# Optimization experiments

Hardware: AMD Instinct MI355X
Metric: run time of the kernel (lower is better)

## Reference

```python
import jax, jax.numpy as jnp
import numpy as np

B, S, D, H, FF = 2, 2048, 1024, 16, 4096
HD = D // H          # head dim = 64
ROT = HD // 2        # rotary dim = dim/(num_heads*2) = 32 (partial rotation)
EPS = 1e-5


def setup_inputs() -> dict:
    key = jax.random.key(0)
    ks = jax.random.split(key, 16)
    std = 0.02
    return {
        "x": jax.random.normal(ks[0], (B, S, D), jnp.float32),
        "mask": jnp.ones((B, 1, 1, S), jnp.int32),
        "wq": jax.random.normal(ks[1], (D, D), jnp.float32) * std,
        "bq": jnp.zeros((D,), jnp.float32),
        "wk": jax.random.normal(ks[2], (D, D), jnp.float32) * std,
        "bk": jnp.zeros((D,), jnp.float32),
        "wv": jax.random.normal(ks[3], (D, D), jnp.float32) * std,
        "bv": jnp.zeros((D,), jnp.float32),
        "wo": jax.random.normal(ks[4], (D, D), jnp.float32) * std,
        "bo": jnp.zeros((D,), jnp.float32),
        "ln1_w": jnp.ones((D,), jnp.float32),
        "ln1_b": jnp.zeros((D,), jnp.float32),
        "ln2_w": jnp.ones((D,), jnp.float32),
        "ln2_b": jnp.zeros((D,), jnp.float32),
        "w1": jax.random.normal(ks[5], (D, FF), jnp.float32) * std,
        "b1": jnp.zeros((FF,), jnp.float32),
        "w2": jax.random.normal(ks[6], (FF, D), jnp.float32) * std,
        "b2": jnp.zeros((D,), jnp.float32),
    }


def _layernorm(x, w, b):
    mu = jnp.mean(x, axis=-1, keepdims=True)
    var = jnp.mean(jnp.square(x - mu), axis=-1, keepdims=True)
    return (x - mu) * jax.lax.rsqrt(var + EPS) * w + b


def _rope(t):
    # t: [B, H, S, HD]; rotate first ROT features, interleaved (GPT-J) pairing
    inv_freq = 1.0 / (10000.0 ** (jnp.arange(0, ROT, 2, dtype=jnp.float32) / ROT))
    ang = jnp.arange(S, dtype=jnp.float32)[:, None] * inv_freq      # [S, ROT//2]
    ang = jnp.repeat(ang, 2, axis=-1)                               # [S, ROT]
    cos, sin = jnp.cos(ang), jnp.sin(ang)
    t_rot, t_pass = t[..., :ROT], t[..., ROT:]
    pr = t_rot.reshape(*t_rot.shape[:-1], ROT // 2, 2)
    rot = jnp.stack([-pr[..., 1], pr[..., 0]], axis=-1).reshape(t_rot.shape)
    return jnp.concatenate([t_rot * cos + rot * sin, t_pass], axis=-1)


def reference(x, mask, wq, bq, wk, bk, wv, bv, wo, bo,
              ln1_w, ln1_b, ln2_w, ln2_b, w1, b1, w2, b2):
    res = x
    h = _layernorm(x, ln1_w, ln1_b)
    q = (h @ wq + bq).reshape(B, S, H, HD).transpose(0, 2, 1, 3)
    k = (h @ wk + bk).reshape(B, S, H, HD).transpose(0, 2, 1, 3)
    v = (h @ wv + bv).reshape(B, S, H, HD).transpose(0, 2, 1, 3)
    q, k = _rope(q), _rope(k)
    score = jnp.einsum('bhqd,bhkd->bhqk', q, k) * (1.0 / np.sqrt(HD))
    score = jnp.where(mask == 0, jnp.float32(-1e9), score)
    attn = jax.nn.softmax(score, axis=-1)
    out = jnp.einsum('bhqk,bhkd->bhqd', attn, v)
    out = out.transpose(0, 2, 1, 3).reshape(B, S, D) @ wo + bo
    x = res + out
    res = x
    h = _layernorm(x, ln2_w, ln2_b)
    h = jax.nn.gelu(h @ w1 + b1, approximate=False) @ w2 + b2
    return res + h
```

## Files before the change

### kernel.cpp

```cpp
#include <hip/hip_runtime.h>
#include <cstdint>
#include <cstddef>


typedef __bf16 bf16;
typedef __bf16 bf16x2 __attribute__((ext_vector_type(2)));
typedef __bf16 bf16x4v __attribute__((ext_vector_type(4)));
typedef __bf16 bf16x8 __attribute__((ext_vector_type(8)));
typedef float  f32x4  __attribute__((ext_vector_type(4)));

#define NB 2
#define NS 2048
#define ND 1024
#define NH 16
#define NHD 64
#define NFF 4096
#define NM (NB*NS)
#define QKSCALE 0.18033688011112042f

typedef uint32_t __attribute__((address_space(1))) gu32_t;
typedef uint32_t __attribute__((address_space(3))) lu32_t;
__device__ __forceinline__ void async_copy16(void* lds, const void* g) {
  __builtin_amdgcn_global_load_lds((gu32_t*)g, (lu32_t*)lds, 16, 0, 0);
}

__device__ __forceinline__ float gelu_f(float x) {
  return 0.5f * x * (1.0f + erff(x * 0.70710678118654752f));
}

__global__ __launch_bounds__(256) void prep_kernel(
    const float* __restrict__ wq, const float* __restrict__ wk,
    const float* __restrict__ wv, const float* __restrict__ wo,
    const float* __restrict__ w1, const float* __restrict__ w2,
    bf16* __restrict__ wqt, bf16* __restrict__ wkt, bf16* __restrict__ wvt,
    bf16* __restrict__ wot, bf16* __restrict__ w1t, bf16* __restrict__ w2t,
    const float* __restrict__ bq, const float* __restrict__ bk,
    const float* __restrict__ bv, float* __restrict__ bcat,
    const int* __restrict__ mask, float* __restrict__ m01f,
    bf16* __restrict__ m01b, float2* __restrict__ rtab,
    const float* __restrict__ x, const float* __restrict__ ln1w,
    const float* __restrict__ ln1b, bf16* __restrict__ h1) {
  int flat = blockIdx.x;
  int t = threadIdx.x;
  if (flat < 12288) {
    __shared__ float tile[32][33];
    const float* W; bf16* Wt; long bx, by; int K, N;
    if (flat < 4096) {
      int which = flat >> 10, r = flat & 1023;
      const float* Ws[4] = {wq, wk, wv, wo};
      bf16* Wts[4] = {wqt, wkt, wvt, wot};
      W = Ws[which]; Wt = Wts[which]; bx = r & 31; by = r >> 5; K = ND; N = ND;
    } else if (flat < 8192) {
      int r = flat - 4096;
      W = w1; Wt = w1t; bx = r & 127; by = r >> 7; K = ND; N = NFF;
    } else {
      int r = flat - 8192;
      W = w2; Wt = w2t; bx = r & 31; by = r >> 5; K = NFF; N = ND;
    }
    int tx = t & 31, ty = t >> 5;
#pragma unroll
    for (int r = 0; r < 4; ++r)
      tile[ty + r*8][tx] = W[(by*32 + ty + r*8) * (long)N + bx*32 + tx];
    __syncthreads();
#pragma unroll
    for (int r = 0; r < 4; ++r)
      Wt[(bx*32 + ty + r*8) * (long)K + by*32 + tx] = (bf16)tile[tx][ty + r*8];
  } else if (flat < 12444) {
    int blk = flat - 12288;
    if (blk < 12) {
      int i = blk * 256 + t;
      bcat[i] = (i < ND) ? bq[i] : ((i < 2*ND) ? bk[i - ND] : bv[i - 2*ND]);
    } else if (blk < 28) {
      int i = (blk - 12) * 256 + t;
      float v = mask[i] ? 1.0f : 0.0f;
      m01f[i] = v;
      m01b[i] = (bf16)v;
    } else {
      int idx = (blk - 28) * 256 + t;
      int s = idx >> 4, i = idx & 15;
      float ang = (float)s * exp2f(-(float)i * (13.287712379549449f / 16.0f));
      float sn, cs;
      sincosf(ang, &sn, &cs);
      rtab[idx] = make_float2(cs, sn);
    }
  } else {
    long row = flat - 12444;
    float4 v = ((const float4*)(x + row*ND))[t];
    float s  = v.x + v.y + v.z + v.w;
    float sq = v.x*v.x + v.y*v.y + v.z*v.z + v.w*v.w;
#pragma unroll
    for (int m = 1; m <= 32; m <<= 1) { s += __shfl_xor(s, m); sq += __shfl_xor(sq, m); }
    __shared__ float ss[4], ssq[4];
    if ((t & 63) == 0) { ss[t>>6] = s; ssq[t>>6] = sq; }
    __syncthreads();
    s  = ss[0] + ss[1] + ss[2] + ss[3];
    sq = ssq[0] + ssq[1] + ssq[2] + ssq[3];
    float mu = s * (1.0f/ND);
    float rs = rsqrtf(sq * (1.0f/ND) - mu*mu + 1e-5f);
    float4 wv4 = ((const float4*)ln1w)[t];
    float4 bv4 = ((const float4*)ln1b)[t];
    bf16x4v o;
    o[0] = (bf16)((v.x-mu)*rs*wv4.x + bv4.x);
    o[1] = (bf16)((v.y-mu)*rs*wv4.y + bv4.y);
    o[2] = (bf16)((v.z-mu)*rs*wv4.z + bv4.z);
    o[3] = (bf16)((v.w-mu)*rs*wv4.w + bv4.w);
    *(bf16x4v*)(h1 + row*ND + t*4) = o;
  }
}

__global__ __launch_bounds__(256) void vtrans_kernel(
    const bf16* __restrict__ v, bf16* __restrict__ vt) {
  __shared__ bf16 t[64][66];
  int st = blockIdx.x, bh = blockIdx.y;
  int b = bh >> 4, h = bh & 15;
  int c = threadIdx.x & 63, rg = threadIdx.x >> 6;
  const bf16* src = v + ((long)b*NS + st*64)*ND + h*64;
#pragma unroll
  for (int i = 0; i < 16; ++i) {
    int r = rg*16 + i;
    t[r][c] = src[(long)r*ND + c];
  }
  __syncthreads();
  bf16* dst = vt + (long)bh*64*NS + st*64;
#pragma unroll
  for (int i = 0; i < 16; ++i) {
    int d = rg*16 + i;
    dst[(long)d*NS + c] = t[c][d];
  }
}

__global__ __launch_bounds__(256) void ln_kernel(
    const float* __restrict__ x, const float* __restrict__ w,
    const float* __restrict__ b, bf16* __restrict__ out) {
  long row = blockIdx.x;
  int t = threadIdx.x;
  float4 v = ((const float4*)(x + row*ND))[t];
  float s  = v.x + v.y + v.z + v.w;
  float sq = v.x*v.x + v.y*v.y + v.z*v.z + v.w*v.w;
#pragma unroll
  for (int m = 1; m <= 32; m <<= 1) { s += __shfl_xor(s, m); sq += __shfl_xor(sq, m); }
  __shared__ float ss[4], ssq[4];
  if ((t & 63) == 0) { ss[t>>6] = s; ssq[t>>6] = sq; }
  __syncthreads();
  s  = ss[0] + ss[1] + ss[2] + ss[3];
  sq = ssq[0] + ssq[1] + ssq[2] + ssq[3];
  float mu = s * (1.0f/ND);
  float rs = rsqrtf(sq * (1.0f/ND) - mu*mu + 1e-5f);
  float4 wv = ((const float4*)w)[t];
  float4 bv = ((const float4*)b)[t];
  bf16x4v o;
  o[0] = (bf16)((v.x-mu)*rs*wv.x + bv.x);
  o[1] = (bf16)((v.y-mu)*rs*wv.y + bv.y);
  o[2] = (bf16)((v.z-mu)*rs*wv.z + bv.z);
  o[3] = (bf16)((v.w-mu)*rs*wv.w + bv.w);
  *(bf16x4v*)(out + row*ND + t*4) = o;
}

__global__ __launch_bounds__(256) void ffn2red_kernel(
    const float* __restrict__ P, const float* __restrict__ y1,
    const float* __restrict__ b2, float* __restrict__ out) {
  const long n4 = (long)NM * ND / 4;
  const float4* p = (const float4*)P;
  const float4* y = (const float4*)y1;
  const float4* bb = (const float4*)b2;
  float4* o = (float4*)out;
  for (long i = (long)blockIdx.x*256 + threadIdx.x; i < n4;
       i += (long)gridDim.x*256) {
    float4 a0 = p[i], a1 = p[i + n4], a2 = p[i + 2*n4], a3 = p[i + 3*n4];
    float4 yv = y[i];
    float4 bv = bb[i & 255];
    float4 r;
    r.x = (a0.x + a1.x) + (a2.x + a3.x) + yv.x + bv.x;
    r.y = (a0.y + a1.y) + (a2.y + a3.y) + yv.y + bv.y;
    r.z = (a0.z + a1.z) + (a2.z + a3.z) + yv.z + bv.z;
    r.w = (a0.w + a1.w) + (a2.w + a3.w) + yv.w + bv.w;
    o[i] = r;
  }
}

template<int EPI>
__global__ __launch_bounds__(512, 2) void gemm256_kernel(
    const bf16* __restrict__ A, const bf16* __restrict__ Bt,
    const float* __restrict__ bias, void* __restrict__ Cout,
    const float2* __restrict__ rtab, const float* __restrict__ m01f,
    int M, int N, int K, int lda, int ldbt) {
  __shared__ __align__(16) bf16 Alds[2][256*64];
  __shared__ __align__(16) bf16 Blds[2][256*64];
  const int tid = threadIdx.x, lane = tid & 63, w = tid >> 6;
  const int fr = lane & 15, kg = lane >> 4;
  const int wr = w >> 2, wc = w & 3;
  const int kz = (EPI == 2) ? blockIdx.z : 0;
  const long kofs = (long)kz * K;

  const int gx = gridDim.x;
  int lin = blockIdx.y * gx + blockIdx.x;
  int nwg = gx * gridDim.y;
  int swz = (lin & 7) * (nwg >> 3) + (lin >> 3);
  const long am0 = (long)(swz / gx) * 256;
  const long bn0 = (long)(swz % gx) * 256;

  const f32x4 fzero = {0.f, 0.f, 0.f, 0.f};
  f32x4 acc[8][4];
#pragma unroll
  for (int m = 0; m < 8; ++m)
#pragma unroll
    for (int n = 0; n < 4; ++n) acc[m][n] = fzero;

  auto stage = [&](int kt, int bufi) {
#pragma unroll
    for (int i = 0; i < 4; ++i) {
      int s = i*512 + tid;
      int r = s >> 3, c = (s & 7) ^ (r & 7);
      async_copy16((char*)&Alds[bufi][0] + i*8192 + w*1024,
                   &A[(am0 + r)*(long)lda + kofs + kt + c*8]);
    }
#pragma unroll
    for (int i = 0; i < 4; ++i) {
      int s = i*512 + tid;
      int r = s >> 3, c = (s & 7) ^ (r & 7);
      async_copy16((char*)&Blds[bufi][0] + i*8192 + w*1024,
                   &Bt[(bn0 + r)*(long)ldbt + kofs + kt + c*8]);
    }
  };

  const int nk = K >> 6;
  stage(0, 0);
  stage(64, 1);
  asm volatile("s_waitcnt vmcnt(8)" ::: "memory");
  __builtin_amdgcn_s_barrier();
  __builtin_amdgcn_sched_barrier(0);

  for (int t = 0; t < nk; ++t) {
    const char* Ab = (const char*)&Alds[t & 1][0];
    const char* Bb = (const char*)&Blds[t & 1][0];
    bf16x8 bfv0[4], bfv1[4], af[4];
#pragma unroll
    for (int n = 0; n < 4; ++n) {
      int r = wc*64 + n*16 + fr;
      bfv0[n] = *(const bf16x8*)(Bb + r*128 + ((kg ^ (r & 7)) << 4));
    }
#pragma unroll
    for (int m = 0; m < 4; ++m) {
      int r = wr*128 + m*16 + fr;
      af[m] = *(const bf16x8*)(Ab + r*128 + ((kg ^ (r & 7)) << 4));
    }
    asm volatile("s_waitcnt lgkmcnt(0)" ::: "memory");
    __builtin_amdgcn_sched_barrier(0);
    __builtin_amdgcn_s_setprio(1);
#pragma unroll
    for (int m = 0; m < 4; ++m)
#pragma unroll
      for (int n = 0; n < 4; ++n)
        acc[m][n] = __builtin_amdgcn_mfma_f32_16x16x32_bf16(af[m], bfv0[n], acc[m][n], 0, 0, 0);
    __builtin_amdgcn_s_setprio(0);
#pragma unroll
    for (int n = 0; n < 4; ++n) {
      int r = wc*64 + n*16 + fr;
      bfv1[n] = *(const bf16x8*)(Bb + r*128 + (((4 + kg) ^ (r & 7)) << 4));
    }
#pragma unroll
    for (int m = 0; m < 4; ++m) {
      int r = wr*128 + m*16 + fr;
      af[m] = *(const bf16x8*)(Ab + r*128 + (((4 + kg) ^ (r & 7)) << 4));
    }
    asm volatile("s_waitcnt lgkmcnt(0)" ::: "memory");
    __builtin_amdgcn_sched_barrier(0);
    __builtin_amdgcn_s_setprio(1);
#pragma unroll
    for (int m = 0; m < 4; ++m)
#pragma unroll
      for (int n = 0; n < 4; ++n)
        acc[m][n] = __builtin_amdgcn_mfma_f32_16x16x32_bf16(af[m], bfv1[n], acc[m][n], 0, 0, 0);
    __builtin_amdgcn_s_setprio(0);
#pragma unroll
    for (int m = 0; m < 4; ++m) {
      int r = wr*128 + (m+4)*16 + fr;
      af[m] = *(const bf16x8*)(Ab + r*128 + ((kg ^ (r & 7)) << 4));
    }
    asm volatile("s_waitcnt lgkmcnt(0)" ::: "memory");
    __builtin_amdgcn_sched_barrier(0);
    __builtin_amdgcn_s_setprio(1);
#pragma unroll
    for (int m = 0; m < 4; ++m)
#pragma unroll
      for (int n = 0; n < 4; ++n)
        acc[m+4][n] = __builtin_amdgcn_mfma_f32_16x16x32_bf16(af[m], bfv0[n], acc[m+4][n], 0, 0, 0);
    __builtin_amdgcn_s_setprio(0);
#pragma unroll
    for (int m = 0; m < 4; ++m) {
      int r = wr*128 + (m+4)*16 + fr;
      af[m] = *(const bf16x8*)(Ab + r*128 + (((4 + kg) ^ (r & 7)) << 4));
    }
    asm volatile("s_waitcnt lgkmcnt(0)" ::: "memory");
    __builtin_amdgcn_sched_barrier(0);
    __builtin_amdgcn_s_setprio(1);
#pragma unroll
    for (int m = 0; m < 4; ++m)
#pragma unroll
      for (int n = 0; n < 4; ++n)
        acc[m+4][n] = __builtin_amdgcn_mfma_f32_16x16x32_bf16(af[m], bfv1[n], acc[m+4][n], 0, 0, 0);
    __builtin_amdgcn_s_setprio(0);

    if (t + 1 == nk) break;
    __builtin_amdgcn_s_barrier();
    __builtin_amdgcn_sched_barrier(0);
    if (t + 2 < nk) {
      stage((t + 2) * 64, t & 1);
      asm volatile("s_waitcnt vmcnt(8)" ::: "memory");
    } else {
      asm volatile("s_waitcnt vmcnt(0)" ::: "memory");
    }
    __builtin_amdgcn_s_barrier();
    __builtin_amdgcn_sched_barrier(0);
  }

  const int rbase = kg * 4;
  const int region = (int)(bn0 >> 10);
#pragma unroll
  for (int m = 0; m < 8; ++m) {
#pragma unroll
    for (int n = 0; n < 4; ++n) {
      long col = bn0 + wc*64 + n*16 + fr;
      float bia = (EPI == 2) ? 0.0f : bias[col];
#pragma unroll
      for (int j = 0; j < 4; ++j) {
        long row = am0 + wr*128 + m*16 + rbase + j;
        float val = acc[m][n][j] + bia;
        if (EPI == 1) {
          ((bf16*)Cout)[row * N + col] = (bf16)gelu_f(val);
        } else if (EPI == 2) {
          ((float*)Cout)[((long)kz * NM + row) * N + col] = val;
        } else {
          long cv = col & 1023;
          if (region <= 1) {
            float pval = __shfl_xor(val, 1);
            if (n < 2) {
              float2 cs = rtab[((row & (NS-1)) << 4) | ((n*16 + fr) >> 1)];
              val = (fr & 1) ? val*cs.x + pval*cs.y : val*cs.x - pval*cs.y;
            }
            if (region == 0) val *= QKSCALE;
          } else {
            val *= m01f[row];
          }
          ((bf16*)Cout)[(long)region * (NM*(long)ND) + row * ND + cv] = (bf16)val;
        }
      }
    }
  }
}

__global__ __launch_bounds__(512, 1) void gemm128x8_kernel(
    const bf16* __restrict__ A, const bf16* __restrict__ Bt,
    const float* __restrict__ bias, const float* __restrict__ res,
    float* __restrict__ Cout, int M, int N, int K) {
  __shared__ __align__(16) bf16 Alds[4][128*64];
  __shared__ __align__(16) bf16 Blds[4][128*64];
  const int tid = threadIdx.x, lane = tid & 63, w = tid >> 6;
  const int fr = lane & 15, kg = lane >> 4;
  const int wr = w >> 1, wc = w & 1;

  const int gx = gridDim.x;
  int lin = blockIdx.y * gx + blockIdx.x;
  int nwg = gx * gridDim.y;
  int swz = (lin & 7) * (nwg >> 3) + (lin >> 3);
  const long am0 = (long)(swz / gx) * 128;
  const long bn0 = (long)(swz % gx) * 128;

  const f32x4 fzero = {0.f, 0.f, 0.f, 0.f};
  f32x4 acc[2][4];
#pragma unroll
  for (int m = 0; m < 2; ++m)
#pragma unroll
    for (int n = 0; n < 4; ++n) acc[m][n] = fzero;

  auto stage = [&](int kt, int bufi) {
#pragma unroll
    for (int i = 0; i < 2; ++i) {
      int s = i*512 + tid;
      int r = s >> 3, c = (s & 7) ^ (r & 7);
      async_copy16((char*)&Alds[bufi][0] + i*8192 + w*1024,
                   &A[(am0 + r)*K + kt + c*8]);
      async_copy16((char*)&Blds[bufi][0] + i*8192 + w*1024,
                   &Bt[(bn0 + r)*K + kt + c*8]);
    }
  };

  const int nk = K >> 6;
  stage(0, 0);
  stage(64, 1);
  asm volatile("s_waitcnt vmcnt(4)" ::: "memory");
  __builtin_amdgcn_s_barrier();
  __builtin_amdgcn_sched_barrier(0);

  for (int t = 0; t < nk; ++t) {
    const int cur = t & 3;
    if (t + 2 < nk) stage((t + 2) * 64, (t + 2) & 3);
    const char* Ab = (const char*)&Alds[cur][0];
    const char* Bb = (const char*)&Blds[cur][0];
    bf16x8 af[2][2], bfv[2][4];
#pragma unroll
    for (int kk = 0; kk < 2; ++kk) {
#pragma unroll
      for (int m = 0; m < 2; ++m) {
        int r = wr*32 + m*16 + fr;
        af[kk][m] = *(const bf16x8*)(Ab + r*128 + (((kk*4 + kg) ^ (r & 7)) << 4));
      }
#pragma unroll
      for (int n = 0; n < 4; ++n) {
        int r = wc*64 + n*16 + fr;
        bfv[kk][n] = *(const bf16x8*)(Bb + r*128 + (((kk*4 + kg) ^ (r & 7)) << 4));
      }
    }
    asm volatile("s_waitcnt lgkmcnt(0)" ::: "memory");
    __builtin_amdgcn_sched_barrier(0);
    __builtin_amdgcn_s_setprio(1);
#pragma unroll
    for (int kk = 0; kk < 2; ++kk)
#pragma unroll
      for (int m = 0; m < 2; ++m)
#pragma unroll
        for (int n = 0; n < 4; ++n)
          acc[m][n] = __builtin_amdgcn_mfma_f32_16x16x32_bf16(af[kk][m], bfv[kk][n], acc[m][n], 0, 0, 0);
    __builtin_amdgcn_s_setprio(0);
    if (t + 2 < nk) { asm volatile("s_waitcnt vmcnt(4)" ::: "memory"); }
    else            { asm volatile("s_waitcnt vmcnt(0)" ::: "memory"); }
    __builtin_amdgcn_s_barrier();
    __builtin_amdgcn_sched_barrier(0);
  }

  const int rbase = kg * 4;
#pragma unroll
  for (int m = 0; m < 2; ++m) {
#pragma unroll
    for (int n = 0; n < 4; ++n) {
      long col = bn0 + wc*64 + n*16 + fr;
      float bia = bias[col];
#pragma unroll
      for (int j = 0; j < 4; ++j) {
        long row = am0 + wr*32 + m*16 + rbase + j;
        Cout[row * N + col] = acc[m][n][j] + bia + res[row * N + col];
      }
    }
  }
}

__global__ __launch_bounds__(512) void attn_kernel(
    const bf16* __restrict__ q, const bf16* __restrict__ k,
    const bf16* __restrict__ vt, const bf16* __restrict__ m01b,
    bf16* __restrict__ out) {
  int lin = blockIdx.y * 16 + blockIdx.x;
  int swz = (lin & 7) * 64 + (lin >> 3);
  const int qt = swz & 15;
  const int bh = swz >> 4;
  const int b = bh >> 4, h = bh & 15;
  const int tid = threadIdx.x, lane = tid & 63, w = tid >> 6;
  const int fr = lane & 15, kg = lane >> 4;
  const int k8 = kg * 8;
  const int frl = fr & 3, frh = fr >> 2;

  __shared__ __align__(16) bf16 Klds[3][64*64];
  __shared__ __align__(16) bf16 Vlds[3][64*64];
  __shared__ __align__(16) bf16 Mlds[NS];

  const long qrow = (long)qt*128 + w*16 + fr;
  const bf16* qbase = q + ((long)b*NS + qrow)*ND + h*NHD;
  bf16x8 qf[2];
  qf[0] = *(const bf16x8*)(qbase + k8);
  qf[1] = *(const bf16x8*)(qbase + 32 + k8);

  const bf16* kbase = k + (long)b*NS*ND + h*NHD;
  const bf16* vtb = vt + (long)bh*64*NS;
  const bf16* mbase = m01b + (long)b*NS;

  if (w < 4) async_copy16((char*)Mlds + w*1024, mbase + tid*8);

  const int srow = tid >> 3, sc = tid & 7;
  const int csK = (sc ^ (srow & 7) ^ (((srow >> 3) & 1) << 2));
  const int csV = (sc ^ (srow & 7));
  auto stageK = [&](int kt, int bufi) {
    async_copy16((char*)&Klds[bufi][0] + w*1024,
                 kbase + ((long)kt*64 + srow)*ND + csK*8);
  };
  auto stageV = [&](int kt, int bufi) {
    async_copy16((char*)&Vlds[bufi][0] + w*1024,
                 vtb + (long)srow*NS + kt*64 + csV*8);
  };

  const f32x4 fzero = {0.f, 0.f, 0.f, 0.f};
  f32x4 oacc[4], oaccL = fzero;
#pragma unroll
  for (int n = 0; n < 4; ++n) oacc[n] = fzero;

  stageK(0, 0); stageV(0, 0);
  stageK(1, 1); stageV(1, 1);
  asm volatile("s_waitcnt vmcnt(2)" ::: "memory");
  __builtin_amdgcn_s_barrier();
  __builtin_amdgcn_sched_barrier(0);

  const int NT = NS / 64;
  int bcur = 0, bpre = 1;
  for (int kt = 0; kt < NT; ++kt) {
    if (kt + 2 < NT) {
      bpre = (bpre == 2) ? 0 : bpre + 1;
      stageK(kt + 2, bpre);
      stageV(kt + 2, bpre);
    }
    const char* Kb = (const char*)&Klds[bcur][0];
    const char* Vb = (const char*)&Vlds[bcur][0];

    bf16x8 vbm0 = *(const bf16x8*)&Mlds[kt*64 + k8];
    bf16x8 vbm1 = *(const bf16x8*)&Mlds[kt*64 + 32 + k8];

    f32x4 sacc[4];
#pragma unroll
    for (int n = 0; n < 4; ++n) sacc[n] = fzero;
#pragma unroll
    for (int n = 0; n < 4; ++n) {
      int r = (frh << 3) + ((n & 1) << 2) + frl + ((n >> 1) << 5);
      int swzr = (r & 7) ^ (((r >> 3) & 1) << 2);
#pragma unroll
      for (int kk = 0; kk < 2; ++kk) {
        bf16x8 kf = *(const bf16x8*)(Kb + r*128 + ((((kk << 2) | kg) ^ swzr) << 4));
        sacc[n] = __builtin_amdgcn_mfma_f32_16x16x32_bf16(kf, qf[kk], sacc[n], 0, 0, 0);
      }
    }

    float p[4][4];
#pragma unroll
    for (int n = 0; n < 4; ++n) {
      p[n][0] = exp2f(sacc[n][0]);
      p[n][1] = exp2f(sacc[n][1]);
      p[n][2] = exp2f(sacc[n][2]);
      p[n][3] = exp2f(sacc[n][3]);
    }

    bf16x8 paf[2];
#pragma unroll
    for (int n = 0; n < 4; ++n) {
#pragma unroll
      for (int j = 0; j < 4; ++j)
        paf[n >> 1][((n & 1) << 2) + j] = (bf16)p[n][j];
    }

    oaccL = __builtin_amdgcn_mfma_f32_16x16x32_bf16(paf[0], vbm0, oaccL, 0, 0, 0);
    oaccL = __builtin_amdgcn_mfma_f32_16x16x32_bf16(paf[1], vbm1, oaccL, 0, 0, 0);

#pragma unroll
    for (int kk = 0; kk < 2; ++kk) {
#pragma unroll
      for (int n2 = 0; n2 < 4; ++n2) {
        int r = n2*16 + fr;
        bf16x8 vb8 = *(const bf16x8*)(Vb + r*128 + ((((kk << 2) | kg) ^ (r & 7)) << 4));
        oacc[n2] = __builtin_amdgcn_mfma_f32_16x16x32_bf16(paf[kk], vb8, oacc[n2], 0, 0, 0);
      }
    }

    if (kt + 2 < NT)      { asm volatile("s_waitcnt vmcnt(2)" ::: "memory"); }
    else if (kt + 1 < NT) { asm volatile("s_waitcnt vmcnt(0)" ::: "memory"); }
    __builtin_amdgcn_s_barrier();
    __builtin_amdgcn_sched_barrier(0);
    bcur = (bcur == 2) ? 0 : bcur + 1;
  }

#pragma unroll
  for (int j = 0; j < 4; ++j) {
    float inv = 1.0f / oaccL[j];
    long orow = (long)qt*128 + w*16 + kg*4 + j;
    bf16* ob = out + ((long)b*NS + orow)*ND + h*NHD;
#pragma unroll
    for (int n2 = 0; n2 < 4; ++n2) ob[n2*16 + fr] = (bf16)(oacc[n2][j] * inv);
  }
}

extern "C" void kernel_launch(void* const* d_in, const int* in_sizes, int n_in,
                              void* d_out, int out_size, void* d_ws, size_t ws_size,
                              hipStream_t stream) {
  const float* x    = (const float*)d_in[0];
  const int*   mask = (const int*)d_in[1];
  const float* wq   = (const float*)d_in[2];
  const float* bq   = (const float*)d_in[3];
  const float* wk   = (const float*)d_in[4];
  const float* bk   = (const float*)d_in[5];
  const float* wv   = (const float*)d_in[6];
  const float* bv   = (const float*)d_in[7];
  const float* wo   = (const float*)d_in[8];
  const float* bo   = (const float*)d_in[9];
  const float* ln1w = (const float*)d_in[10];
  const float* ln1b = (const float*)d_in[11];
  const float* ln2w = (const float*)d_in[12];
  const float* ln2b = (const float*)d_in[13];
  const float* w1   = (const float*)d_in[14];
  const float* b1   = (const float*)d_in[15];
  const float* w2   = (const float*)d_in[16];
  const float* b2   = (const float*)d_in[17];
  float* out = (float*)d_out;

  char* ws = (char*)d_ws;
  const size_t MB = 1024ull * 1024ull;
  bf16* wqt = (bf16*)(ws + 0*MB);
  bf16* wkt = (bf16*)(ws + 2*MB);
  bf16* wvt = (bf16*)(ws + 4*MB);
  bf16* wot = (bf16*)(ws + 6*MB);
  bf16* w1t = (bf16*)(ws + 8*MB);
  bf16* w2t = (bf16*)(ws + 16*MB);
  bf16* h1   = (bf16*)(ws + 24*MB);
  bf16* qb   = (bf16*)(ws + 32*MB);
  bf16* kb   = (bf16*)(ws + 40*MB);
  bf16* vb   = (bf16*)(ws + 48*MB);
  bf16* vtb  = h1;
  bf16* attnb = (bf16*)(ws + 72*MB);
  bf16* f1   = (bf16*)(ws + 24*MB);
  float* y1  = (float*)(ws + 56*MB);
  bf16* h2   = (bf16*)(ws + 72*MB);
  float* bcat = (float*)(ws + 80*MB);
  float* m01f = (float*)(ws + 80*MB + 16*1024);
  bf16*  m01b = (bf16*) (ws + 80*MB + 32*1024);
  float2* rtab = (float2*)(ws + 80*MB + 48*1024);
  float* pK   = (float*)(ws + 84*MB);
  const bool use_splitk = (ws_size >= 148ull*MB);
  (void)in_sizes; (void)n_in; (void)out_size;

  prep_kernel<<<16540, 256, 0, stream>>>(wq, wk, wv, wo, w1, w2,
                                         wqt, wkt, wvt, wot, w1t, w2t,
                                         bq, bk, bv, bcat, mask, m01f, m01b,
                                         rtab, x, ln1w, ln1b, h1);

  gemm256_kernel<3><<<dim3(12, 16), 512, 0, stream>>>(h1, wqt, bcat, qb,
                                                      rtab, m01f, NM, 3*ND, ND,
                                                      ND, ND);
  vtrans_kernel<<<dim3(32, 32), 256, 0, stream>>>(vb, vtb);

  attn_kernel<<<dim3(16, 32), 512, 0, stream>>>(qb, kb, vtb, m01b, attnb);

  gemm128x8_kernel<<<dim3(8, 32), 512, 0, stream>>>(attnb, wot, bo, x, y1,
                                                    NM, ND, ND);
  ln_kernel<<<NM, 256, 0, stream>>>(y1, ln2w, ln2b, h2);
  gemm256_kernel<1><<<dim3(16, 16), 512, 0, stream>>>(h2, w1t, b1, f1,
                                                      nullptr, nullptr,
                                                      NM, NFF, ND, ND, ND);
  if (use_splitk) {
    gemm256_kernel<2><<<dim3(4, 16, 4), 512, 0, stream>>>(f1, w2t, nullptr, pK,
                                                          nullptr, nullptr,
                                                          NM, ND, ND, NFF, NFF);
    ffn2red_kernel<<<2048, 256, 0, stream>>>(pK, y1, b2, out);
  } else {
    gemm128x8_kernel<<<dim3(8, 32), 512, 0, stream>>>(f1, w2t, b2, y1, out,
                                                      NM, ND, NFF);
  }
}
```

Measured before the change: 274.2 us.

## Store split-K FFN2 partials in bf16 and precompute attention LDS offsets

The split-K FFN2 GEMM now writes its four partial sums as bf16 instead of fp32, and the reduction kernel reads them eight at a time. This halves the partial-buffer traffic and lowers the workspace threshold needed to enable split-K. The attention kernel also precomputes its swizzled LDS read offsets and uses incrementing global pointers for staging, which cuts per-iteration address arithmetic. Rounding the partials to bf16 before summing adds some precision loss in the FFN output.

```diff
diff --git a/kernel.cpp b/kernel.cpp
--- a/kernel.cpp
+++ b/kernel.cpp
@@ -157,24 +157,31 @@
 }
 
 __global__ __launch_bounds__(256) void ffn2red_kernel(
-    const float* __restrict__ P, const float* __restrict__ y1,
+    const bf16* __restrict__ P, const float* __restrict__ y1,
     const float* __restrict__ b2, float* __restrict__ out) {
-  const long n4 = (long)NM * ND / 4;
-  const float4* p = (const float4*)P;
-  const float4* y = (const float4*)y1;
-  const float4* bb = (const float4*)b2;
-  float4* o = (float4*)out;
-  for (long i = (long)blockIdx.x*256 + threadIdx.x; i < n4;
+  const long n8 = (long)NM * ND / 8;
+  for (long i = (long)blockIdx.x*256 + threadIdx.x; i < n8;
        i += (long)gridDim.x*256) {
-    float4 a0 = p[i], a1 = p[i + n4], a2 = p[i + 2*n4], a3 = p[i + 3*n4];
-    float4 yv = y[i];
-    float4 bv = bb[i & 255];
-    float4 r;
-    r.x = (a0.x + a1.x) + (a2.x + a3.x) + yv.x + bv.x;
-    r.y = (a0.y + a1.y) + (a2.y + a3.y) + yv.y + bv.y;
-    r.z = (a0.z + a1.z) + (a2.z + a3.z) + yv.z + bv.z;
-    r.w = (a0.w + a1.w) + (a2.w + a3.w) + yv.w + bv.w;
-    o[i] = r;
+    bf16x8 p0 = ((const bf16x8*)P)[i];
+    bf16x8 p1 = ((const bf16x8*)P)[i + n8];
+    bf16x8 p2 = ((const bf16x8*)P)[i + 2*n8];
+    bf16x8 p3 = ((const bf16x8*)P)[i + 3*n8];
+    float4 ya = ((const float4*)y1)[2*i];
+    float4 yb = ((const float4*)y1)[2*i + 1];
+    int cb = (int)((i * 8) & 1023);
+    float4 ba = *(const float4*)&b2[cb];
+    float4 bb = *(const float4*)&b2[cb + 4];
+    float4 ra, rb;
+    ra.x = ((float)p0[0]+(float)p1[0])+((float)p2[0]+(float)p3[0]) + ya.x + ba.x;
+    ra.y = ((float)p0[1]+(float)p1[1])+((float)p2[1]+(float)p3[1]) + ya.y + ba.y;
+    ra.z = ((float)p0[2]+(float)p1[2])+((float)p2[2]+(float)p3[2]) + ya.z + ba.z;
+    ra.w = ((float)p0[3]+(float)p1[3])+((float)p2[3]+(float)p3[3]) + ya.w + ba.w;
+    rb.x = ((float)p0[4]+(float)p1[4])+((float)p2[4]+(float)p3[4]) + yb.x + bb.x;
+    rb.y = ((float)p0[5]+(float)p1[5])+((float)p2[5]+(float)p3[5]) + yb.y + bb.y;
+    rb.z = ((float)p0[6]+(float)p1[6])+((float)p2[6]+(float)p3[6]) + yb.z + bb.z;
+    rb.w = ((float)p0[7]+(float)p1[7])+((float)p2[7]+(float)p3[7]) + yb.w + bb.w;
+    ((float4*)out)[2*i]     = ra;
+    ((float4*)out)[2*i + 1] = rb;
   }
 }
 
@@ -329,7 +336,7 @@
         if (EPI == 1) {
           ((bf16*)Cout)[row * N + col] = (bf16)gelu_f(val);
         } else if (EPI == 2) {
-          ((float*)Cout)[((long)kz * NM + row) * N + col] = val;
+          ((bf16*)Cout)[((long)kz * NM + row) * N + col] = (bf16)val;
         } else {
           long cv = col & 1023;
           if (region <= 1) {
@@ -474,36 +481,55 @@
 
   if (w < 4) async_copy16((char*)Mlds + w*1024, mbase + tid*8);
 
+  int offK[4][2], offV[2][4];
+#pragma unroll
+  for (int n = 0; n < 4; ++n) {
+    int r = (frh << 3) + ((n & 1) << 2) + frl + ((n >> 1) << 5);
+    int swzr = (r & 7) ^ (((r >> 3) & 1) << 2);
+#pragma unroll
+    for (int kk = 0; kk < 2; ++kk)
+      offK[n][kk] = r*128 + ((((kk << 2) | kg) ^ swzr) << 4);
+  }
+#pragma unroll
+  for (int kk = 0; kk < 2; ++kk)
+#pragma unroll
+    for (int n2 = 0; n2 < 4; ++n2) {
+      int r = n2*16 + fr;
+      offV[kk][n2] = r*128 + ((((kk << 2) | kg) ^ (r & 7)) << 4);
+    }
+
   const int srow = tid >> 3, sc = tid & 7;
   const int csK = (sc ^ (srow & 7) ^ (((srow >> 3) & 1) << 2));
   const int csV = (sc ^ (srow & 7));
-  auto stageK = [&](int kt, int bufi) {
-    async_copy16((char*)&Klds[bufi][0] + w*1024,
-                 kbase + ((long)kt*64 + srow)*ND + csK*8);
-  };
-  auto stageV = [&](int kt, int bufi) {
-    async_copy16((char*)&Vlds[bufi][0] + w*1024,
-                 vtb + (long)srow*NS + kt*64 + csV*8);
-  };
+  const bf16* kp0 = kbase + (long)srow*ND + csK*8;
+  const bf16* vp0 = vtb + (long)srow*NS + csV*8;
+  const int ldsoff = w*1024;
 
   const f32x4 fzero = {0.f, 0.f, 0.f, 0.f};
   f32x4 oacc[4], oaccL = fzero;
 #pragma unroll
   for (int n = 0; n < 4; ++n) oacc[n] = fzero;
 
-  stageK(0, 0); stageV(0, 0);
-  stageK(1, 1); stageV(1, 1);
+  async_copy16((char*)&Klds[0][0] + ldsoff, kp0);
+  async_copy16((char*)&Vlds[0][0] + ldsoff, vp0);
+  async_copy16((char*)&Klds[1][0] + ldsoff, kp0 + 64*ND);
+  async_copy16((char*)&Vlds[1][0] + ldsoff, vp0 + 64);
   asm volatile("s_waitcnt vmcnt(2)" ::: "memory");
   __builtin_amdgcn_s_barrier();
   __builtin_amdgcn_sched_barrier(0);
+
+  const bf16* kp = kp0 + 2L*64*ND;
+  const bf16* vp = vp0 + 2*64;
 
   const int NT = NS / 64;
   int bcur = 0, bpre = 1;
   for (int kt = 0; kt < NT; ++kt) {
     if (kt + 2 < NT) {
       bpre = (bpre == 2) ? 0 : bpre + 1;
-      stageK(kt + 2, bpre);
-      stageV(kt + 2, bpre);
+      async_copy16((char*)&Klds[bpre][0] + ldsoff, kp);
+      async_copy16((char*)&Vlds[bpre][0] + ldsoff, vp);
+      kp += 64*ND;
+      vp += 64;
     }
     const char* Kb = (const char*)&Klds[bcur][0];
     const char* Vb = (const char*)&Vlds[bcur][0];
@@ -516,11 +542,9 @@
     for (int n = 0; n < 4; ++n) sacc[n] = fzero;
 #pragma unroll
     for (int n = 0; n < 4; ++n) {
-      int r = (frh << 3) + ((n & 1) << 2) + frl + ((n >> 1) << 5);
-      int swzr = (r & 7) ^ (((r >> 3) & 1) << 2);
 #pragma unroll
       for (int kk = 0; kk < 2; ++kk) {
-        bf16x8 kf = *(const bf16x8*)(Kb + r*128 + ((((kk << 2) | kg) ^ swzr) << 4));
+        bf16x8 kf = *(const bf16x8*)(Kb + offK[n][kk]);
         sacc[n] = __builtin_amdgcn_mfma_f32_16x16x32_bf16(kf, qf[kk], sacc[n], 0, 0, 0);
       }
     }
@@ -549,8 +573,7 @@
     for (int kk = 0; kk < 2; ++kk) {
 #pragma unroll
       for (int n2 = 0; n2 < 4; ++n2) {
-        int r = n2*16 + fr;
-        bf16x8 vb8 = *(const bf16x8*)(Vb + r*128 + ((((kk << 2) | kg) ^ (r & 7)) << 4));
+        bf16x8 vb8 = *(const bf16x8*)(Vb + offV[kk][n2]);
         oacc[n2] = __builtin_amdgcn_mfma_f32_16x16x32_bf16(paf[kk], vb8, oacc[n2], 0, 0, 0);
       }
     }
@@ -616,8 +639,8 @@
   float* m01f = (float*)(ws + 80*MB + 16*1024);
   bf16*  m01b = (bf16*) (ws + 80*MB + 32*1024);
   float2* rtab = (float2*)(ws + 80*MB + 48*1024);
-  float* pK   = (float*)(ws + 84*MB);
-  const bool use_splitk = (ws_size >= 148ull*MB);
+  bf16* pK   = (bf16*)(ws + 84*MB);
+  const bool use_splitk = (ws_size >= 116ull*MB);
   (void)in_sizes; (void)n_in; (void)out_size;
 
   prep_kernel<<<16540, 256, 0, stream>>>(wq, wk, wv, wo, w1, w2,
```

Result: faster. 266.6 us (-2.8%).
